# Kernel optimization log

Hardware: AMD Instinct MI355X
Metric: run time of the kernel (lower is better)

Reference implementation:

```python
import jax, jax.numpy as jnp
import numpy as np

N_NODES = 50000
N_EDGES = 800000
FEAT = 128
HID = 128
CONCAT = 2
OUT_CH = 64
NUM_CL = [[12, 8, 5], [12, 8, 5]]
N_TASKS = 2


def setup_inputs() -> dict:
    key = jax.random.key(0)
    ks = iter(jax.random.split(key, 64))
    s = 0.05

    def w(shape):
        return jax.random.normal(next(ks), shape, dtype=jnp.float32) * s

    inp = {}
    inp["X"] = jax.random.normal(next(ks), (N_TASKS, CONCAT, N_NODES, FEAT), dtype=jnp.float32)
    inp["edge_src"] = jax.random.randint(next(ks), (N_EDGES,), 0, N_NODES, dtype=jnp.int32)
    inp["edge_dst"] = jax.random.randint(next(ks), (N_EDGES,), 0, N_NODES, dtype=jnp.int32)
    inp["y"] = jax.random.randint(next(ks), (N_TASKS, N_NODES, 3), 0, 5, dtype=jnp.int32)

    # LASAGE encoder params (SAGEConv: lin_l (agg, with bias) + lin_r (root, no bias))
    inp["Wl_i0"], inp["bl_i0"], inp["Wr_i0"] = w((FEAT, HID)), w((HID,)), w((FEAT, HID))
    inp["Wl_i1"], inp["bl_i1"], inp["Wr_i1"] = w((FEAT, HID)), w((HID,)), w((FEAT, HID))
    mid = CONCAT * HID  # 256
    inp["Wl_m"], inp["bl_m"], inp["Wr_m"] = w((mid, mid)), w((mid,)), w((mid, mid))
    inp["Wl_o"], inp["bl_o"], inp["Wr_o"] = w((mid, OUT_CH)), w((OUT_CH,)), w((mid, OUT_CH))

    # Task heads, stacked over tasks (same shape per head type across tasks)
    c0, c1, c2 = NUM_CL[0]
    inp["Wl_mt"], inp["bl_mt"], inp["Wr_mt"] = w((N_TASKS, OUT_CH, c0)), w((N_TASKS, c0)), w((N_TASKS, OUT_CH, c0))
    inp["Wl_mt2"], inp["bl_mt2"], inp["Wr_mt2"] = w((N_TASKS, OUT_CH, c1)), w((N_TASKS, c1)), w((N_TASKS, OUT_CH, c1))
    inp["Wl_mt3"], inp["bl_mt3"], inp["Wr_mt3"] = w((N_TASKS, OUT_CH, c2)), w((N_TASKS, c2)), w((N_TASKS, OUT_CH, c2))
    return inp


def reference(X, edge_src, edge_dst, y,
              Wl_i0, bl_i0, Wr_i0, Wl_i1, bl_i1, Wr_i1,
              Wl_m, bl_m, Wr_m, Wl_o, bl_o, Wr_o,
              Wl_mt, bl_mt, Wr_mt, Wl_mt2, bl_mt2, Wr_mt2, Wl_mt3, bl_mt3, Wr_mt3):
    n = X.shape[2]
    deg = jax.ops.segment_sum(jnp.ones_like(edge_dst, dtype=X.dtype), edge_dst, num_segments=n)
    inv_deg = (1.0 / jnp.maximum(deg, 1.0))[:, None]

    def sage(x, Wl, bl, Wr):
        # mean-aggregate neighbor features, then lin_l(agg) + lin_r(x)
        agg = jax.ops.segment_sum(x[edge_src], edge_dst, num_segments=n) * inv_deg
        return agg @ Wl + bl + x @ Wr

    def ce(logits, labels):
        logp = jax.nn.log_softmax(logits, axis=-1)
        return -jnp.mean(jnp.take_along_axis(logp, labels[:, None].astype(jnp.int32), axis=1))

    loss = jnp.float32(0.0)
    for k in range(X.shape[0]):
        # LASAGE encoder (eval mode: dropout inactive)
        h0 = jax.nn.relu(sage(X[k, 0], Wl_i0, bl_i0, Wr_i0))
        h1 = jax.nn.relu(sage(X[k, 1], Wl_i1, bl_i1, Wr_i1))
        xk = jnp.concatenate([h0, h1], axis=-1)  # [N, 256]
        xk = jax.nn.relu(sage(xk, Wl_m, bl_m, Wr_m))
        hk = jax.nn.sigmoid(sage(xk, Wl_o, bl_o, Wr_o))  # [N, 64]
        # per-task heads, sigmoid applied before CE (faithful to source)
        o0 = jax.nn.sigmoid(sage(hk, Wl_mt[k], bl_mt[k], Wr_mt[k]))
        o1 = jax.nn.sigmoid(sage(hk, Wl_mt2[k], bl_mt2[k], Wr_mt2[k]))
        o2 = jax.nn.sigmoid(sage(hk, Wl_mt3[k], bl_mt3[k], Wr_mt3[k]))
        loss = loss + ce(o0, y[k, :, 0]) + ce(o1, y[k, :, 1]) + ce(o2, y[k, :, 2])
    return loss
```

## Files before the change

### kernel.cpp

```cpp
#include <hip/hip_runtime.h>
#include <math.h>

#define NN 50000
#define NE 800000

typedef short bf16x8 __attribute__((ext_vector_type(8)));
typedef float f32x4 __attribute__((ext_vector_type(4)));
typedef float f32x2 __attribute__((ext_vector_type(2)));

__device__ inline ushort f2bf(float f) {
    union { float f; uint u; } v; v.f = f;
    uint r = v.u + 0x7FFFu + ((v.u >> 16) & 1u);
    return (ushort)(r >> 16);
}
__device__ inline float bf2f(ushort h) {
    union { uint u; float f; } v; v.u = ((uint)h) << 16;
    return v.f;
}
__device__ inline uchar f2fp8(float f) {
    float a = fminf(fabsf(f), 448.f);
    union { float f; uint u; } v; v.f = a * 7.52316384526264e-37f;
    uint r = (v.u + 0x7FFFFu + ((v.u >> 20) & 1u)) >> 20;
    if (r > 0x7Eu) r = 0x7Eu;
    union { float f; uint u; } s; s.f = f;
    return (uchar)(r | ((s.u >> 31) << 7));
}
__device__ inline float fp8dec(uint b) {
    union { uint u; float f; } t; t.u = (b & 0x7Fu) << 20;
    union { float f; uint u; } o; o.f = t.f * 1.3292279957849159e36f;
    o.u |= (b & 0x80u) << 24;
    return o.f;
}
__device__ inline void acc_fp8x4(float* acc, uint u) {
#if __has_builtin(__builtin_amdgcn_cvt_pk_f32_fp8)
    f32x2 lo = __builtin_amdgcn_cvt_pk_f32_fp8((int)u, false);
    f32x2 hi = __builtin_amdgcn_cvt_pk_f32_fp8((int)u, true);
    acc[0] += lo[0]; acc[1] += lo[1]; acc[2] += hi[0]; acc[3] += hi[1];
#else
    acc[0] += fp8dec(u & 0xFFu);
    acc[1] += fp8dec((u >> 8) & 0xFFu);
    acc[2] += fp8dec((u >> 16) & 0xFFu);
    acc[3] += fp8dec(u >> 24);
#endif
}
__device__ inline uint pk2bf(float a, float b) {
    return (uint)f2bf(a) | ((uint)f2bf(b) << 16);
}
__device__ inline uint pk4f8(float a, float b, float c, float d) {
    return (uint)f2fp8(a) | ((uint)f2fp8(b) << 8) | ((uint)f2fp8(c) << 16) | ((uint)f2fp8(d) << 24);
}


__global__ void count_edges_k(const int* __restrict__ edst, int* __restrict__ counts, int e) {
    int i = blockIdx.x * blockDim.x + threadIdx.x;
    if (i < e) atomicAdd(&counts[edst[i]], 1);
}

__global__ __launch_bounds__(1024) void scan1_k(const int* __restrict__ counts,
                                                int* __restrict__ row_start,
                                                int* __restrict__ bsum, int n) {
    __shared__ int sd[1024];
    int i = blockIdx.x * 1024 + threadIdx.x;
    int v = (i < n) ? counts[i] : 0;
    sd[threadIdx.x] = v;
    __syncthreads();
    for (int off = 1; off < 1024; off <<= 1) {
        int t = (threadIdx.x >= off) ? sd[threadIdx.x - off] : 0;
        __syncthreads();
        sd[threadIdx.x] += t;
        __syncthreads();
    }
    if (i < n) row_start[i] = sd[threadIdx.x] - v;
    if (threadIdx.x == 1023) bsum[blockIdx.x] = sd[1023];
}

__global__ void scan2_k(int* __restrict__ bsum, int nb) {
    int lane = threadIdx.x;
    int v = (lane < nb) ? bsum[lane] : 0;
    int orig = v;
    for (int off = 1; off < 64; off <<= 1) {
        int t = __shfl_up(v, off);
        if (lane >= off) v += t;
    }
    if (lane < nb) bsum[lane] = v - orig;
}

__global__ void scan3_k(const int* __restrict__ counts, const int* __restrict__ bsum,
                        int* __restrict__ row_start, int* __restrict__ cursor,
                        float* __restrict__ inv_deg, int n, int e) {
    int i = blockIdx.x * blockDim.x + threadIdx.x;
    if (i < n) {
        int rs = row_start[i] + bsum[i >> 10];
        row_start[i] = rs;
        cursor[i] = rs;
        inv_deg[i] = 1.0f / fmaxf((float)counts[i], 1.0f);
        if (i == 0) row_start[n] = e;
    }
}

__global__ void fill_csr_k(const int* __restrict__ esrc, const int* __restrict__ edst,
                           int* __restrict__ cursor, int* __restrict__ csr_src, int e) {
    int i = blockIdx.x * blockDim.x + threadIdx.x;
    if (i < e) {
        int pos = atomicAdd(&cursor[edst[i]], 1);
        csr_src[pos] = esrc[i];
    }
}


__global__ void prep_w_k(const float* __restrict__ W1, const float* __restrict__ W2,
                         ushort* __restrict__ Wt, int K, int M) {
    int i = blockIdx.x * blockDim.x + threadIdx.x;
    int tot = 2 * M * K;
    if (i >= tot) return;
    int c = i / K, k = i - c * K;
    float v = (c < M) ? W1[(size_t)k * M + c] : W2[(size_t)k * M + (c - M)];
    Wt[i] = f2bf(v);
}


struct GArg { const void* A; const ushort* Wt; uchar* V8; ushort* R; };
template<int NY> struct GArgs { GArg a[NY]; };

template<bool A_FP32, int NY>
__global__ __launch_bounds__(256) void gemm_mfma_k(GArgs<NY> P, int K, int M,
                                                   int ldv, int ldr, int n) {
    __shared__ __align__(16) ushort As[64 * 40];
    __shared__ __align__(16) ushort Bs[128 * 40];
    const GArg& G = P.a[blockIdx.z];
    const void* __restrict__ Av = G.A;
    const ushort* __restrict__ Wt = G.Wt;

    int tid = threadIdx.x;
    int row0 = blockIdx.x * 64;
    int col0 = blockIdx.y * 128;
    int lane = tid & 63, wid = tid >> 6;
    int wm = wid & 1, wn = wid >> 1;
    int lrow = lane & 15, lko = (lane >> 4) * 8;

    f32x4 acc[2][4];
    #pragma unroll
    for (int i = 0; i < 2; ++i)
        #pragma unroll
        for (int j = 0; j < 4; ++j)
            acc[i][j] = (f32x4){0.f, 0.f, 0.f, 0.f};

    for (int kc = 0; kc < K; kc += 32) {
        __syncthreads();
        if constexpr (A_FP32) {
            const float* A = (const float*)Av;
            #pragma unroll
            for (int l = tid; l < 512; l += 256) {
                int r = l >> 3, s = l & 7;
                int rg = row0 + r;
                float4 a = (rg < n) ? *(const float4*)(A + (size_t)rg * K + kc + s * 4)
                                    : make_float4(0.f, 0.f, 0.f, 0.f);
                ushort* dst = &As[r * 40 + s * 4];
                dst[0] = f2bf(a.x); dst[1] = f2bf(a.y); dst[2] = f2bf(a.z); dst[3] = f2bf(a.w);
            }
        } else {
            const ushort* A = (const ushort*)Av;
            int r = tid >> 2, s = tid & 3;
            int rg = row0 + r;
            uint4 a = (rg < n) ? *(const uint4*)(A + (size_t)rg * K + kc + s * 8)
                               : make_uint4(0u, 0u, 0u, 0u);
            *(uint4*)(&As[r * 40 + s * 8]) = a;
        }
        #pragma unroll
        for (int l = tid; l < 512; l += 256) {
            int r = l >> 2, s = l & 3;
            int cg = col0 + r;
            *(uint4*)(&Bs[r * 40 + s * 8]) = *(const uint4*)(Wt + (size_t)cg * K + kc + s * 8);
        }
        __syncthreads();

        bf16x8 af[2], bfr[4];
        #pragma unroll
        for (int i = 0; i < 2; ++i)
            af[i] = *(const bf16x8*)(&As[(wm * 32 + i * 16 + lrow) * 40 + lko]);
        #pragma unroll
        for (int j = 0; j < 4; ++j)
            bfr[j] = *(const bf16x8*)(&Bs[(wn * 64 + j * 16 + lrow) * 40 + lko]);
        #pragma unroll
        for (int i = 0; i < 2; ++i)
            #pragma unroll
            for (int j = 0; j < 4; ++j)
                acc[i][j] = __builtin_amdgcn_mfma_f32_16x16x32_bf16(af[i], bfr[j], acc[i][j], 0, 0, 0);
    }

    #pragma unroll
    for (int i = 0; i < 2; ++i) {
        int rbase = row0 + wm * 32 + i * 16 + (lane >> 4) * 4;
        #pragma unroll
        for (int j = 0; j < 4; ++j) {
            int cg = col0 + wn * 64 + j * 16 + lrow;
            #pragma unroll
            for (int q = 0; q < 4; ++q) {
                int rg = rbase + q;
                if (rg < n) {
                    float v = acc[i][j][q];
                    if (cg < M) G.V8[(size_t)rg * ldv + cg] = f2fp8(v);
                    else        G.R[(size_t)rg * ldr + (cg - M)] = f2bf(v);
                }
            }
        }
    }
}


struct Bias4 { const float* b[4]; };

template<int NZ, int U>
__global__ __launch_bounds__(256) void agg_f512_k(const uchar* __restrict__ V8,
                                                  const ushort* __restrict__ R,
                                                  Bias4 B,
                                                  const float* __restrict__ inv_deg,
                                                  const int* __restrict__ row_start,
                                                  const int* __restrict__ csr_src,
                                                  ushort* __restrict__ xkout,
                                                  size_t tstride, int n) {
    constexpr int LPZ = 64 / NZ;
    int wid  = (blockIdx.x * blockDim.x + threadIdx.x) >> 6;
    int lane = threadIdx.x & 63;
    if (wid >= n) return;
    int dst = wid;
    int c0 = (lane & (LPZ - 1)) * 8;
    const float* bp = B.b[lane / LPZ] + c0;
    int off8 = lane * 8;

    float acc[8];
    #pragma unroll
    for (int q = 0; q < 8; ++q) acc[q] = 0.f;

    int s = row_start[dst], e = row_start[dst + 1];
    for (int g = s; g < e; g += U) {
        int idx[U];
        #pragma unroll
        for (int u = 0; u < U; ++u)
            idx[u] = (g + u < e) ? csr_src[g + u] : -1;
        uint2 d[U];
        #pragma unroll
        for (int u = 0; u < U; ++u) {
            d[u] = make_uint2(0u, 0u);
            if (idx[u] >= 0) d[u] = *(const uint2*)(V8 + (size_t)idx[u] * 512 + off8);
        }
        #pragma unroll
        for (int u = 0; u < U; ++u) {
            acc_fp8x4(acc,     d[u].x);
            acc_fp8x4(acc + 4, d[u].y);
        }
    }

    float inv = inv_deg[dst];
    float r[8];
    uint4 rr = *(const uint4*)(R + (size_t)dst * 512 + off8);
    uint rw[4] = {rr.x, rr.y, rr.z, rr.w};
    #pragma unroll
    for (int q = 0; q < 8; ++q) r[q] = acc[q] * inv + bp[q];
    #pragma unroll
    for (int p = 0; p < 4; ++p) {
        r[p * 2 + 0] += bf2f((ushort)(rw[p] & 0xFFFF));
        r[p * 2 + 1] += bf2f((ushort)(rw[p] >> 16));
    }
    #pragma unroll
    for (int q = 0; q < 8; ++q) r[q] = fmaxf(r[q], 0.f);

    uint4 o;
    o.x = pk2bf(r[0], r[1]); o.y = pk2bf(r[2], r[3]);
    o.z = pk2bf(r[4], r[5]); o.w = pk2bf(r[6], r[7]);
    *(uint4*)(xkout + (size_t)(lane >> 5) * tstride + (size_t)dst * 256 + (lane & 31) * 8) = o;
}


template<int ACT, bool WF8, int U>
__global__ __launch_bounds__(256) void agg_f128_k(const uchar* __restrict__ V8,
                                                  const ushort* __restrict__ R,
                                                  const float* __restrict__ bias,
                                                  const float* __restrict__ inv_deg,
                                                  const int* __restrict__ row_start,
                                                  const int* __restrict__ csr_src,
                                                  ushort* __restrict__ outb, size_t tstride,
                                                  uchar* __restrict__ out8,
                                                  int n) {
    int wid  = (blockIdx.x * blockDim.x + threadIdx.x) >> 6;
    int lane = threadIdx.x & 63;
    if (wid >= n) return;
    int dst   = wid;
    int sub   = lane & 15;
    int eslot = lane >> 4;
    int task  = sub >> 3;
    int c0    = (sub & 7) * 8;

    float acc[8];
    #pragma unroll
    for (int q = 0; q < 8; ++q) acc[q] = 0.f;

    int s = row_start[dst], e = row_start[dst + 1];
    for (int g = s; g < e; g += 4 * U) {
        int idx[U];
        #pragma unroll
        for (int u = 0; u < U; ++u) {
            int t = g + u * 4 + eslot;
            idx[u] = (t < e) ? csr_src[t] : -1;
        }
        uint2 d[U];
        #pragma unroll
        for (int u = 0; u < U; ++u) {
            d[u] = make_uint2(0u, 0u);
            if (idx[u] >= 0) d[u] = *(const uint2*)(V8 + (size_t)idx[u] * 128 + sub * 8);
        }
        #pragma unroll
        for (int u = 0; u < U; ++u) {
            acc_fp8x4(acc,     d[u].x);
            acc_fp8x4(acc + 4, d[u].y);
        }
    }

    #pragma unroll
    for (int mask = 16; mask < 64; mask <<= 1)
        #pragma unroll
        for (int q = 0; q < 8; ++q)
            acc[q] += __shfl_xor(acc[q], mask);

    if (eslot == 0) {
        float inv = inv_deg[dst];
        float r[8];
        #pragma unroll
        for (int q = 0; q < 8; ++q) r[q] = acc[q] * inv;
        if (bias) {
            #pragma unroll
            for (int q = 0; q < 8; ++q) r[q] += bias[c0 + q];
        }
        if (R) {
            uint4 rr = *(const uint4*)(R + (size_t)dst * 128 + sub * 8);
            uint rw[4] = {rr.x, rr.y, rr.z, rr.w};
            #pragma unroll
            for (int p = 0; p < 4; ++p) {
                r[p * 2 + 0] += bf2f((ushort)(rw[p] & 0xFFFF));
                r[p * 2 + 1] += bf2f((ushort)(rw[p] >> 16));
            }
        }
        #pragma unroll
        for (int q = 0; q < 8; ++q) {
            if constexpr (ACT == 2) r[q] = 1.f / (1.f + expf(-r[q]));
        }
        uint4 o;
        o.x = pk2bf(r[0], r[1]); o.y = pk2bf(r[2], r[3]);
        o.z = pk2bf(r[4], r[5]); o.w = pk2bf(r[6], r[7]);
        *(uint4*)(outb + (size_t)task * tstride + (size_t)dst * 64 + c0) = o;
        if constexpr (WF8) {
            uint2 o8;
            o8.x = pk4f8(r[0], r[1], r[2], r[3]);
            o8.y = pk4f8(r[4], r[5], r[6], r[7]);
            *(uint2*)(out8 + (size_t)dst * 128 + sub * 8) = o8;
        }
    }
}


template<int C>
__device__ inline float ce_from_z(float* z, int label) {
    float m = -1e30f;
    #pragma unroll
    for (int c = 0; c < C; ++c) { z[c] = 1.f / (1.f + expf(-z[c])); m = fmaxf(m, z[c]); }
    float ssum = 0.f, zl = 0.f;
    #pragma unroll
    for (int c = 0; c < C; ++c) { ssum += expf(z[c] - m); if (c == label) zl = z[c]; }
    return (logf(ssum) + m) - zl;
}

__global__ __launch_bounds__(256) void head_ce_k(const ushort* __restrict__ Ah,
                                                 const ushort* __restrict__ hk,
                                                 const float* __restrict__ Wl1, const float* __restrict__ b1, const float* __restrict__ Wr1,
                                                 const float* __restrict__ Wl2, const float* __restrict__ b2, const float* __restrict__ Wr2,
                                                 const float* __restrict__ Wl3, const float* __restrict__ b3, const float* __restrict__ Wr3,
                                                 const int* __restrict__ yv,
                                                 float* __restrict__ loss_acc, int n) {
    int ty = blockIdx.y;
    int nidx = blockIdx.x * blockDim.x + threadIdx.x;
    Wl1 += ty * 64 * 12; b1 += ty * 12; Wr1 += ty * 64 * 12;
    Wl2 += ty * 64 * 8;  b2 += ty * 8;  Wr2 += ty * 64 * 8;
    Wl3 += ty * 64 * 5;  b3 += ty * 5;  Wr3 += ty * 64 * 5;
    float lsum = 0.f;
    if (nidx < n) {
        float z0[12], z1[8], z2[5];
        #pragma unroll
        for (int c = 0; c < 12; ++c) z0[c] = b1[c];
        #pragma unroll
        for (int c = 0; c < 8; ++c) z1[c] = b2[c];
        #pragma unroll
        for (int c = 0; c < 5; ++c) z2[c] = b3[c];

        const ushort* ap = Ah + ((size_t)ty * NN + nidx) * 64;
        const ushort* hp = hk + ((size_t)ty * NN + nidx) * 64;
        for (int d8 = 0; d8 < 64; d8 += 8) {
            uint4 ua = *(const uint4*)(ap + d8);
            uint4 uh = *(const uint4*)(hp + d8);
            uint aw[4] = {ua.x, ua.y, ua.z, ua.w};
            uint hw[4] = {uh.x, uh.y, uh.z, uh.w};
            #pragma unroll
            for (int p = 0; p < 4; ++p) {
                #pragma unroll
                for (int half = 0; half < 2; ++half) {
                    int d = d8 + p * 2 + half;
                    float av = bf2f((ushort)(half ? (aw[p] >> 16) : (aw[p] & 0xFFFF)));
                    float hv = bf2f((ushort)(half ? (hw[p] >> 16) : (hw[p] & 0xFFFF)));
                    #pragma unroll
                    for (int c = 0; c < 12; ++c)
                        z0[c] = fmaf(av, Wl1[d * 12 + c], fmaf(hv, Wr1[d * 12 + c], z0[c]));
                    #pragma unroll
                    for (int c = 0; c < 8; ++c)
                        z1[c] = fmaf(av, Wl2[d * 8 + c], fmaf(hv, Wr2[d * 8 + c], z1[c]));
                    #pragma unroll
                    for (int c = 0; c < 5; ++c)
                        z2[c] = fmaf(av, Wl3[d * 5 + c], fmaf(hv, Wr3[d * 5 + c], z2[c]));
                }
            }
        }
        const int* yp = yv + ((size_t)ty * NN + nidx) * 3;
        lsum  = ce_from_z<12>(z0, yp[0]);
        lsum += ce_from_z<8 >(z1, yp[1]);
        lsum += ce_from_z<5 >(z2, yp[2]);
    }
    for (int off = 32; off > 0; off >>= 1) lsum += __shfl_down(lsum, off);
    __shared__ float ssum[4];
    int wv = threadIdx.x >> 6, ln = threadIdx.x & 63;
    if (ln == 0) ssum[wv] = lsum;
    __syncthreads();
    if (threadIdx.x == 0) atomicAdd(loss_acc, ssum[0] + ssum[1] + ssum[2] + ssum[3]);
}

__global__ void finalize_k(const float* __restrict__ loss_acc, float* __restrict__ out, int n) {
    out[0] = loss_acc[0] * (1.0f / (float)n);
}


extern "C" void kernel_launch(void* const* d_in, const int* in_sizes, int n_in,
                              void* d_out, int out_size, void* d_ws, size_t ws_size,
                              hipStream_t stream) {
    const float* X    = (const float*)d_in[0];
    const int*   esrc = (const int*)d_in[1];
    const int*   edst = (const int*)d_in[2];
    const int*   y    = (const int*)d_in[3];
    const float* Wl_i[2] = {(const float*)d_in[4], (const float*)d_in[7]};
    const float* bl_i[2] = {(const float*)d_in[5], (const float*)d_in[8]};
    const float* Wr_i[2] = {(const float*)d_in[6], (const float*)d_in[9]};
    const float* Wl_m = (const float*)d_in[10], *bl_m = (const float*)d_in[11], *Wr_m = (const float*)d_in[12];
    const float* Wl_o = (const float*)d_in[13], *bl_o = (const float*)d_in[14], *Wr_o = (const float*)d_in[15];
    const float* Wl_t1 = (const float*)d_in[16], *bl_t1 = (const float*)d_in[17], *Wr_t1 = (const float*)d_in[18];
    const float* Wl_t2 = (const float*)d_in[19], *bl_t2 = (const float*)d_in[20], *Wr_t2 = (const float*)d_in[21];
    const float* Wl_t3 = (const float*)d_in[22], *bl_t3 = (const float*)d_in[23], *Wr_t3 = (const float*)d_in[24];

    const int N = NN, E = NE;
    char* p = (char*)d_ws;
    auto alloc = [&](size_t bytes) -> char* {
        char* r = p;
        p += (bytes + 255) & ~(size_t)255;
        return r;
    };
    int*    counts    = (int*)alloc((size_t)N * 4);
    int*    row_start = (int*)alloc((size_t)(N + 1) * 4);
    int*    cursor    = (int*)alloc((size_t)N * 4);
    int*    bsum      = (int*)alloc(64 * 4);
    int*    csr_src   = (int*)alloc((size_t)E * 4);
    float*  inv_deg   = (float*)alloc((size_t)N * 4);
    float*  loss_acc  = (float*)alloc(256);
    uchar*  V8i  = (uchar*)alloc((size_t)N * 512);
    ushort* Ri   = (ushort*)alloc((size_t)N * 512 * 2);
    uchar*  V8m  = (uchar*)alloc((size_t)N * 512);
    ushort* Rm   = (ushort*)alloc((size_t)N * 512 * 2);
    uchar*  V8o  = (uchar*)alloc((size_t)N * 128);
    ushort* Ro   = (ushort*)alloc((size_t)N * 128 * 2);
    ushort* xk   = (ushort*)alloc((size_t)2 * N * 256 * 2);
    ushort* hk   = (ushort*)alloc((size_t)2 * N * 64 * 2);
    uchar*  hk8  = (uchar*)alloc((size_t)N * 128);
    ushort* Ah   = (ushort*)alloc((size_t)2 * N * 64 * 2);
    ushort* Wt_i0 = (ushort*)alloc((size_t)256 * 128 * 2);
    ushort* Wt_i1 = (ushort*)alloc((size_t)256 * 128 * 2);
    ushort* Wt_m  = (ushort*)alloc((size_t)512 * 256 * 2);
    ushort* Wt_o  = (ushort*)alloc((size_t)128 * 256 * 2);

    hipMemsetAsync(counts, 0, (size_t)N * 4, stream);
    hipMemsetAsync(loss_acc, 0, 4, stream);
    count_edges_k<<<(E + 255) / 256, 256, 0, stream>>>(edst, counts, E);
    const int NB = (N + 1023) / 1024;
    scan1_k<<<NB, 1024, 0, stream>>>(counts, row_start, bsum, N);
    scan2_k<<<1, 64, 0, stream>>>(bsum, NB);
    scan3_k<<<(N + 255) / 256, 256, 0, stream>>>(counts, bsum, row_start, cursor, inv_deg, N, E);
    fill_csr_k<<<(E + 255) / 256, 256, 0, stream>>>(esrc, edst, cursor, csr_src, E);

    prep_w_k<<<(2 * 128 * 128 + 255) / 256, 256, 0, stream>>>(Wl_i[0], Wr_i[0], Wt_i0, 128, 128);
    prep_w_k<<<(2 * 128 * 128 + 255) / 256, 256, 0, stream>>>(Wl_i[1], Wr_i[1], Wt_i1, 128, 128);
    prep_w_k<<<(2 * 256 * 256 + 255) / 256, 256, 0, stream>>>(Wl_m, Wr_m, Wt_m, 256, 256);
    prep_w_k<<<(2 * 256 * 64 + 255) / 256, 256, 0, stream>>>(Wl_o, Wr_o, Wt_o, 256, 64);

    const int RB = (N + 63) / 64;
    const int AGB = (N + 3) / 4;
    const ushort* Wt_i[2] = {Wt_i0, Wt_i1};
    const size_t TSX = (size_t)N * 256;
    const size_t TSH = (size_t)N * 64;

    {
        GArgs<4> P;
        for (int z = 0; z < 4; ++z)
            P.a[z] = {X + (size_t)z * N * 128, Wt_i[z & 1], V8i + z * 128, Ri + z * 128};
        gemm_mfma_k<true, 4><<<dim3(RB, 2, 4), 256, 0, stream>>>(P, 128, 128, 512, 512, N);
    }
    {
        Bias4 B = {{bl_i[0], bl_i[1], bl_i[0], bl_i[1]}};
        agg_f512_k<4, 4><<<AGB, 256, 0, stream>>>(V8i, Ri, B, inv_deg, row_start, csr_src,
                                                  xk, TSX, N);
    }
    {
        GArgs<2> P;
        for (int k = 0; k < 2; ++k)
            P.a[k] = {xk + (size_t)k * TSX, Wt_m, V8m + k * 256, Rm + k * 256};
        gemm_mfma_k<false, 2><<<dim3(RB, 4, 2), 256, 0, stream>>>(P, 256, 256, 512, 512, N);
    }
    {
        Bias4 B = {{bl_m, bl_m, nullptr, nullptr}};
        agg_f512_k<2, 4><<<AGB, 256, 0, stream>>>(V8m, Rm, B, inv_deg, row_start, csr_src,
                                                  xk, TSX, N);
    }
    {
        GArgs<2> P;
        for (int k = 0; k < 2; ++k)
            P.a[k] = {xk + (size_t)k * TSX, Wt_o, V8o + k * 64, Ro + k * 64};
        gemm_mfma_k<false, 2><<<dim3(RB, 1, 2), 256, 0, stream>>>(P, 256, 64, 128, 128, N);
    }
    agg_f128_k<2, true, 2><<<AGB, 256, 0, stream>>>(V8o, Ro, bl_o, inv_deg, row_start, csr_src,
                                                    hk, TSH, hk8, N);
    agg_f128_k<0, false, 2><<<AGB, 256, 0, stream>>>(hk8, nullptr, nullptr, inv_deg, row_start, csr_src,
                                                     Ah, TSH, nullptr, N);
    head_ce_k<<<dim3((N + 255) / 256, 2), 256, 0, stream>>>(Ah, hk,
        Wl_t1, bl_t1, Wr_t1, Wl_t2, bl_t2, Wr_t2, Wl_t3, bl_t3, Wr_t3,
        y, loss_acc, N);

    finalize_k<<<1, 1, 0, stream>>>(loss_acc, (float*)d_out, N);
}
```

Baseline: 516.2 us.

## Prefetch next GEMM tile into registers and stage epilogue stores through LDS

The MFMA GEMM now loads the next K-chunk of A and W into registers while the current chunk is computed, so global-load latency overlaps with the matrix ops. The epilogue writes fp8 and bf16 results into shared memory first and then issues coalesced 16-byte global stores, replacing scattered per-element byte and short stores. This adds register pressure and extra barriers, and the mixed-column branch assumes M=64 with a 128-wide tile.

New measurement: 500.2 us. 3.1% less time.

```diff
diff --git a/kernel.cpp b/kernel.cpp
--- a/kernel.cpp
+++ b/kernel.cpp
@@ -125,8 +125,9 @@
 template<bool A_FP32, int NY>
 __global__ __launch_bounds__(256) void gemm_mfma_k(GArgs<NY> P, int K, int M,
                                                    int ldv, int ldr, int n) {
-    __shared__ __align__(16) ushort As[64 * 40];
-    __shared__ __align__(16) ushort Bs[128 * 40];
+    __shared__ __align__(16) uchar smem[16384];
+    ushort* As = (ushort*)smem;
+    ushort* Bs = As + 64 * 40;
     const GArg& G = P.a[blockIdx.z];
     const void* __restrict__ Av = G.A;
     const ushort* __restrict__ Wt = G.Wt;
@@ -145,34 +146,52 @@
         for (int j = 0; j < 4; ++j)
             acc[i][j] = (f32x4){0.f, 0.f, 0.f, 0.f};
 
-    for (int kc = 0; kc < K; kc += 32) {
-        __syncthreads();
+    float4 fA0, fA1;
+    uint4 uA, uB0, uB1;
+
+    auto LOAD = [&](int kc) {
         if constexpr (A_FP32) {
             const float* A = (const float*)Av;
-            #pragma unroll
-            for (int l = tid; l < 512; l += 256) {
-                int r = l >> 3, s = l & 7;
-                int rg = row0 + r;
-                float4 a = (rg < n) ? *(const float4*)(A + (size_t)rg * K + kc + s * 4)
-                                    : make_float4(0.f, 0.f, 0.f, 0.f);
-                ushort* dst = &As[r * 40 + s * 4];
-                dst[0] = f2bf(a.x); dst[1] = f2bf(a.y); dst[2] = f2bf(a.z); dst[3] = f2bf(a.w);
-            }
+            int r = tid >> 3, s = tid & 7;
+            int rg0 = row0 + r, rg1 = rg0 + 32;
+            fA0 = (rg0 < n) ? *(const float4*)(A + (size_t)rg0 * K + kc + s * 4)
+                            : make_float4(0.f, 0.f, 0.f, 0.f);
+            fA1 = (rg1 < n) ? *(const float4*)(A + (size_t)rg1 * K + kc + s * 4)
+                            : make_float4(0.f, 0.f, 0.f, 0.f);
         } else {
             const ushort* A = (const ushort*)Av;
             int r = tid >> 2, s = tid & 3;
             int rg = row0 + r;
-            uint4 a = (rg < n) ? *(const uint4*)(A + (size_t)rg * K + kc + s * 8)
-                               : make_uint4(0u, 0u, 0u, 0u);
-            *(uint4*)(&As[r * 40 + s * 8]) = a;
-        }
-        #pragma unroll
-        for (int l = tid; l < 512; l += 256) {
-            int r = l >> 2, s = l & 3;
-            int cg = col0 + r;
-            *(uint4*)(&Bs[r * 40 + s * 8]) = *(const uint4*)(Wt + (size_t)cg * K + kc + s * 8);
-        }
+            uA = (rg < n) ? *(const uint4*)(A + (size_t)rg * K + kc + s * 8)
+                          : make_uint4(0u, 0u, 0u, 0u);
+        }
+        int rB = tid >> 2, sB = tid & 3;
+        uB0 = *(const uint4*)(Wt + (size_t)(col0 + rB) * K + kc + sB * 8);
+        uB1 = *(const uint4*)(Wt + (size_t)(col0 + rB + 64) * K + kc + sB * 8);
+    };
+    auto STORE_LDS = [&]() {
+        if constexpr (A_FP32) {
+            int r = tid >> 3, s = tid & 7;
+            ushort* d0 = &As[r * 40 + s * 4];
+            d0[0] = f2bf(fA0.x); d0[1] = f2bf(fA0.y); d0[2] = f2bf(fA0.z); d0[3] = f2bf(fA0.w);
+            ushort* d1 = &As[(r + 32) * 40 + s * 4];
+            d1[0] = f2bf(fA1.x); d1[1] = f2bf(fA1.y); d1[2] = f2bf(fA1.z); d1[3] = f2bf(fA1.w);
+        } else {
+            int r = tid >> 2, s = tid & 3;
+            *(uint4*)(&As[r * 40 + s * 8]) = uA;
+        }
+        int rB = tid >> 2, sB = tid & 3;
+        *(uint4*)(&Bs[rB * 40 + sB * 8]) = uB0;
+        *(uint4*)(&Bs[(rB + 64) * 40 + sB * 8]) = uB1;
+    };
+
+    const int nIt = K >> 5;
+    LOAD(0);
+    for (int it = 0; it < nIt; ++it) {
         __syncthreads();
+        STORE_LDS();
+        __syncthreads();
+        if (it + 1 < nIt) LOAD((it + 1) << 5);
 
         bf16x8 af[2], bfr[4];
         #pragma unroll
@@ -188,21 +207,70 @@
                 acc[i][j] = __builtin_amdgcn_mfma_f32_16x16x32_bf16(af[i], bfr[j], acc[i][j], 0, 0, 0);
     }
 
-    #pragma unroll
-    for (int i = 0; i < 2; ++i) {
-        int rbase = row0 + wm * 32 + i * 16 + (lane >> 4) * 4;
-        #pragma unroll
-        for (int j = 0; j < 4; ++j) {
-            int cg = col0 + wn * 64 + j * 16 + lrow;
+    __syncthreads();
+    if (col0 + 128 <= M) {
+        uchar* C8 = (uchar*)smem;
+        #pragma unroll
+        for (int i = 0; i < 2; ++i) {
+            int lr0 = wm * 32 + i * 16 + (lane >> 4) * 4;
             #pragma unroll
-            for (int q = 0; q < 4; ++q) {
-                int rg = rbase + q;
-                if (rg < n) {
-                    float v = acc[i][j][q];
-                    if (cg < M) G.V8[(size_t)rg * ldv + cg] = f2fp8(v);
-                    else        G.R[(size_t)rg * ldr + (cg - M)] = f2bf(v);
+            for (int j = 0; j < 4; ++j) {
+                int lc = wn * 64 + j * 16 + lrow;
+                #pragma unroll
+                for (int q = 0; q < 4; ++q)
+                    C8[(lr0 + q) * 128 + lc] = f2fp8(acc[i][j][q]);
+            }
+        }
+        __syncthreads();
+        int row = tid >> 2, seg = tid & 3;
+        if (row0 + row < n) {
+            uint4* g = (uint4*)(G.V8 + (size_t)(row0 + row) * ldv + col0 + seg * 32);
+            const uint4* s4 = (const uint4*)(C8 + row * 128 + seg * 32);
+            g[0] = s4[0]; g[1] = s4[1];
+        }
+    } else if (col0 >= M) {
+        ushort* C16 = (ushort*)smem;
+        #pragma unroll
+        for (int i = 0; i < 2; ++i) {
+            int lr0 = wm * 32 + i * 16 + (lane >> 4) * 4;
+            #pragma unroll
+            for (int j = 0; j < 4; ++j) {
+                int lc = wn * 64 + j * 16 + lrow;
+                #pragma unroll
+                for (int q = 0; q < 4; ++q)
+                    C16[(lr0 + q) * 128 + lc] = f2bf(acc[i][j][q]);
+            }
+        }
+        __syncthreads();
+        int row = tid >> 2, seg = tid & 3;
+        if (row0 + row < n) {
+            uint4* g = (uint4*)(G.R + (size_t)(row0 + row) * ldr + (col0 - M) + seg * 32);
+            const uint4* s4 = (const uint4*)((const uchar*)C16 + row * 256 + seg * 64);
+            g[0] = s4[0]; g[1] = s4[1]; g[2] = s4[2]; g[3] = s4[3];
+        }
+    } else {
+        uchar*  C8  = (uchar*)smem;
+        ushort* C16 = (ushort*)(smem + 4096);
+        #pragma unroll
+        for (int i = 0; i < 2; ++i) {
+            int lr0 = wm * 32 + i * 16 + (lane >> 4) * 4;
+            #pragma unroll
+            for (int j = 0; j < 4; ++j) {
+                int lc = j * 16 + lrow;
+                #pragma unroll
+                for (int q = 0; q < 4; ++q) {
+                    if (wn == 0) C8[(lr0 + q) * 64 + lc] = f2fp8(acc[i][j][q]);
+                    else         C16[(lr0 + q) * 64 + lc] = f2bf(acc[i][j][q]);
                 }
             }
+        }
+        __syncthreads();
+        int row = tid >> 2, seg = tid & 3;
+        if (row0 + row < n) {
+            *(uint4*)(G.V8 + (size_t)(row0 + row) * ldv + seg * 16) =
+                *(const uint4*)(C8 + row * 64 + seg * 16);
+            *(uint4*)(G.R + (size_t)(row0 + row) * ldr + seg * 16) =
+                *(const uint4*)((const uchar*)C16 + row * 128 + seg * 32);
         }
     }
 }
```
